# Performance work log

Measured on AMD Instinct MI355X. Metric: run time of the kernel, lower is better.

The kernel has to match this reference:

```python
import jax, jax.numpy as jnp
import numpy as np

NEG = -1e9

def setup_inputs() -> dict:
    key = jax.random.key(0)
    k1, k2, k3, k4, k5 = jax.random.split(key, 5)
    B, S, D = 4, 2048, 1024
    x = jax.random.normal(k1, (B, S, D), dtype=jnp.float32)
    Wq = jax.random.normal(k2, (D, D), dtype=jnp.float32) * (1.0 / np.sqrt(D))
    Wk = jax.random.normal(k3, (D, D), dtype=jnp.float32) * (1.0 / np.sqrt(D))
    Wv = jax.random.normal(k4, (D, D), dtype=jnp.float32) * (1.0 / np.sqrt(D))
    mask = jax.random.randint(k5, (B, S), 0, 2) > 0  # bool [B,S]
    return {"x": x, "Wq": Wq, "Wk": Wk, "Wv": Wv, "mask": mask}

def reference(x, Wq, Wk, Wv, mask):
    # x: [B,S,D]; single-head self-attention, scale = 1/sqrt(D)
    D = x.shape[-1]
    scale = 1.0 / D ** 0.5
    q = jnp.einsum('bsi,ij->bsj', x, Wq)
    k = jnp.einsum('bsi,ij->bsj', x, Wk)
    y = jnp.einsum('bsi,bzi->bsz', q, k) * scale  # [B,S,S]
    # additive mask: (~mask)[:, :, None] * -1e9 broadcasts over key axis
    m = (~mask).astype(jnp.float32)[:, :, None]
    y = y + m * NEG
    v = jnp.einsum('bsi,ij->bsj', x, Wv)
    attn = jax.nn.softmax(y, axis=-1)
    return jnp.einsum('bsz,bzi->bsi', attn, v)
```

## Files before the change

### kernel.cpp

```cpp
#include <hip/hip_runtime.h>

typedef __bf16 bf16x8 __attribute__((ext_vector_type(8)));
typedef float f32x4 __attribute__((ext_vector_type(4)));
typedef unsigned short u16;

__device__ __forceinline__ u16 f2bf(float f) {
    union { float f; unsigned u; } v; v.f = f;
    unsigned r = (v.u + 0x7FFFu + ((v.u >> 16) & 1u)) >> 16;
    return (u16)r;
}

__global__ __launch_bounds__(256)
void normMask(const unsigned int* __restrict__ m, unsigned char* __restrict__ nm) {
    __shared__ int isByte;
    if (threadIdx.x == 0) isByte = 0;
    __syncthreads();
    int bad = 0;
    for (int i = threadIdx.x; i < 2048; i += 256) bad |= (m[i] > 1u);
    if (bad) atomicOr(&isByte, 1);
    __syncthreads();
    if (isByte) {
        const unsigned char* mb = (const unsigned char*)m;
        for (int i = threadIdx.x; i < 8192; i += 256) nm[i] = mb[i] ? 1 : 0;
    } else {
        for (int i = threadIdx.x; i < 8192; i += 256) nm[i] = (unsigned char)m[i];
    }
}

__global__ __launch_bounds__(256)
void transW(const float* __restrict__ Wq, const float* __restrict__ Wk,
            const float* __restrict__ Wv, u16* __restrict__ Wt) {
    __shared__ u16 tile[64][65];
    const float* W = blockIdx.z == 0 ? Wq : (blockIdx.z == 1 ? Wk : Wv);
    u16* out = Wt + (size_t)blockIdx.z * 1024 * 1024;
    int k0 = blockIdx.x * 64, n0 = blockIdx.y * 64;
    int t = threadIdx.x, cl = t & 63, rw = t >> 6;
    #pragma unroll
    for (int r = 0; r < 16; ++r) {
        int row = r * 4 + rw;
        tile[cl][row] = f2bf(W[(size_t)(k0 + row) * 1024 + n0 + cl]);
    }
    __syncthreads();
    #pragma unroll
    for (int r = 0; r < 16; ++r) {
        int row = r * 4 + rw;
        out[(size_t)(n0 + row) * 1024 + k0 + cl] = tile[row][cl];
    }
}

__global__ __launch_bounds__(256)
void convX(const float* __restrict__ x, u16* __restrict__ xb) {
    const size_t n4 = (size_t)8192 * 1024 / 4;
    for (size_t i = (size_t)blockIdx.x * 256 + threadIdx.x; i < n4; i += (size_t)gridDim.x * 256) {
        float4 v = ((const float4*)x)[i];
        ushort4 o = make_ushort4(f2bf(v.x), f2bf(v.y), f2bf(v.z), f2bf(v.w));
        ((ushort4*)xb)[i] = o;
    }
}

__global__ __launch_bounds__(256)
void transV(const u16* __restrict__ qkv, u16* __restrict__ vt) {
    __shared__ u16 tile[64][65];
    int b = blockIdx.z;
    int s0 = blockIdx.x * 64, d0 = blockIdx.y * 64;
    int t = threadIdx.x, cl = t & 63, rw = t >> 6;
    const u16* src = qkv + (size_t)b * 2048 * 3072 + 2048;
    #pragma unroll
    for (int r = 0; r < 16; ++r) {
        int row = r * 4 + rw;
        tile[cl][row] = src[(size_t)(s0 + row) * 3072 + d0 + cl];
    }
    __syncthreads();
    u16* dst = vt + (size_t)b * 1024 * 2048;
    #pragma unroll
    for (int r = 0; r < 16; ++r) {
        int row = r * 4 + rw;
        dst[(size_t)(d0 + row) * 2048 + s0 + cl] = tile[row][cl];
    }
}

template <int OUTV>
__global__ __launch_bounds__(256, 2)
void gemm_bt(const u16* __restrict__ A0, int lda, size_t sA,
             const u16* __restrict__ B0, int ldb, size_t sB,
             void* __restrict__ Cout, int ldc, size_t sC, int kdim) {
    __shared__ u16 lA[128 * 64];
    __shared__ u16 lB[128 * 64];
    const u16* A = A0 + (size_t)blockIdx.z * sA;
    const u16* B = B0 + (size_t)blockIdx.z * sB;
    const int t = threadIdx.x;
    const int w = t >> 6, l = t & 63;
    const int wr = w >> 1, wc = w & 1;
    const int brow = blockIdx.x * 128, bcol = blockIdx.y * 128;
    const int rt = l >> 3;
    const int cb = (l & 7) * 8;

    auto ldsA3 = (__attribute__((address_space(3))) char*)lA;
    auto ldsB3 = (__attribute__((address_space(3))) char*)lB;

    f32x4 acc[4][4];
    #pragma unroll
    for (int m = 0; m < 4; ++m)
        #pragma unroll
        for (int n = 0; n < 4; ++n)
            acc[m][n] = (f32x4){0.f, 0.f, 0.f, 0.f};

    for (int k0 = 0; k0 < kdim; k0 += 64) {
        __syncthreads();
        #pragma unroll
        for (int p = 0; p < 4; ++p) {
            int chunk = p * 4 + w;
            const u16* ga = A + (size_t)(brow + chunk * 8 + rt) * lda + k0 + cb;
            __builtin_amdgcn_global_load_lds(
                (const __attribute__((address_space(1))) void*)ga,
                (__attribute__((address_space(3))) void*)(ldsA3 + chunk * 1024), 16, 0, 0);
            const u16* gb = B + (size_t)(bcol + chunk * 8 + rt) * ldb + k0 + cb;
            __builtin_amdgcn_global_load_lds(
                (const __attribute__((address_space(1))) void*)gb,
                (__attribute__((address_space(3))) void*)(ldsB3 + chunk * 1024), 16, 0, 0);
        }
        __syncthreads();
        #pragma unroll
        for (int kk = 0; kk < 2; ++kk) {
            bf16x8 af[4], bfv[4];
            #pragma unroll
            for (int m = 0; m < 4; ++m)
                af[m] = *(const bf16x8*)&lA[(wr * 64 + m * 16 + (l & 15)) * 64 + kk * 32 + (l >> 4) * 8];
            #pragma unroll
            for (int n = 0; n < 4; ++n)
                bfv[n] = *(const bf16x8*)&lB[(wc * 64 + n * 16 + (l & 15)) * 64 + kk * 32 + (l >> 4) * 8];
            #pragma unroll
            for (int m = 0; m < 4; ++m)
                #pragma unroll
                for (int n = 0; n < 4; ++n)
                    acc[m][n] = __builtin_amdgcn_mfma_f32_16x16x32_bf16(af[m], bfv[n], acc[m][n], 0, 0, 0);
        }
    }

    const int lrow = (l >> 4) * 4, lcol = l & 15;
    #pragma unroll
    for (int m = 0; m < 4; ++m) {
        #pragma unroll
        for (int n = 0; n < 4; ++n) {
            int rr = brow + wr * 64 + m * 16 + lrow;
            int cc = bcol + wc * 64 + n * 16 + lcol;
            #pragma unroll
            for (int j = 0; j < 4; ++j) {
                if constexpr (OUTV == 0)
                    ((u16*)Cout)[(size_t)blockIdx.z * sC + (size_t)(rr + j) * ldc + cc] = f2bf(acc[m][n][j]);
                else
                    ((float*)Cout)[(size_t)blockIdx.z * sC + (size_t)(rr + j) * ldc + cc] = acc[m][n][j];
            }
        }
    }
}

__global__ __launch_bounds__(256)
void softmax_rows(const float* __restrict__ S0, size_t sS, u16* __restrict__ P0, size_t sP,
                  const unsigned char* __restrict__ nm, int bbase) {
    const int row = blockIdx.x, t = threadIdx.x;
    const int b = bbase + blockIdx.z;
    const float* S = S0 + (size_t)blockIdx.z * sS;
    u16* dst = P0 + (size_t)blockIdx.z * sP + (size_t)row * 2048;
    if (nm[b * 2048 + row] == 0) {
        ushort4 u = make_ushort4(0x3A00, 0x3A00, 0x3A00, 0x3A00);
        ((ushort4*)dst)[t] = u;
        ((ushort4*)dst)[t + 256] = u;
        return;
    }
    const float4* src = (const float4*)(S + (size_t)row * 2048);
    float4 a = src[t], c = src[t + 256];
    float v[8] = {a.x, a.y, a.z, a.w, c.x, c.y, c.z, c.w};
    float mx = -1e30f;
    #pragma unroll
    for (int i = 0; i < 8; ++i) { v[i] *= 0.03125f; mx = fmaxf(mx, v[i]); }
    #pragma unroll
    for (int o = 32; o > 0; o >>= 1) mx = fmaxf(mx, __shfl_xor(mx, o));
    __shared__ float redm[4], reds[4];
    if ((t & 63) == 0) redm[t >> 6] = mx;
    __syncthreads();
    mx = fmaxf(fmaxf(redm[0], redm[1]), fmaxf(redm[2], redm[3]));
    float s = 0.f;
    #pragma unroll
    for (int i = 0; i < 8; ++i) { v[i] = expf(v[i] - mx); s += v[i]; }
    #pragma unroll
    for (int o = 32; o > 0; o >>= 1) s += __shfl_xor(s, o);
    if ((t & 63) == 0) reds[t >> 6] = s;
    __syncthreads();
    s = (reds[0] + reds[1]) + (reds[2] + reds[3]);
    float inv = 1.0f / s;
    ushort4 o0 = make_ushort4(f2bf(v[0] * inv), f2bf(v[1] * inv), f2bf(v[2] * inv), f2bf(v[3] * inv));
    ushort4 o1 = make_ushort4(f2bf(v[4] * inv), f2bf(v[5] * inv), f2bf(v[6] * inv), f2bf(v[7] * inv));
    ((ushort4*)dst)[t] = o0;
    ((ushort4*)dst)[t + 256] = o1;
}

extern "C" void kernel_launch(void* const* d_in, const int* in_sizes, int n_in,
                              void* d_out, int out_size, void* d_ws, size_t ws_size,
                              hipStream_t stream) {
    const float* x  = (const float*)d_in[0];
    const float* Wq = (const float*)d_in[1];
    const float* Wk = (const float*)d_in[2];
    const float* Wv = (const float*)d_in[3];
    const unsigned int* mask = (const unsigned int*)d_in[4];
    float* out = (float*)d_out;

    char* p = (char*)d_ws;
    u16* Wt  = (u16*)p;  p += (size_t)3072 * 1024 * 2;
    u16* xb  = (u16*)p;  p += (size_t)8192 * 1024 * 2;
    u16* qkv = (u16*)p;  p += (size_t)8192 * 3072 * 2;
    u16* vt  = (u16*)p;  p += (size_t)4 * 1024 * 2048 * 2;
    char* base = p;
    const size_t sizeS = (size_t)2048 * 2048 * 4;
    const size_t sizeP = (size_t)2048 * 2048 * 2;
    bool batched = ws_size >= (size_t)(base - (char*)d_ws) + 4 * (sizeS + sizeP) + 8192;

    float* S = (float*)base;
    u16* P;
    unsigned char* nm;
    if (batched) {
        P  = (u16*)(base + 4 * sizeS);
        nm = (unsigned char*)(base + 4 * (sizeS + sizeP));
    } else {
        P  = (u16*)(base + sizeS);
        nm = (unsigned char*)(base + sizeS + sizeP);
    }

    normMask<<<1, 256, 0, stream>>>(mask, nm);
    transW<<<dim3(16, 16, 3), 256, 0, stream>>>(Wq, Wk, Wv, Wt);
    convX<<<2048, 256, 0, stream>>>(x, xb);
    gemm_bt<0><<<dim3(64, 24, 1), 256, 0, stream>>>(xb, 1024, 0, Wt, 1024, 0, qkv, 3072, 0, 1024);
    transV<<<dim3(32, 16, 4), 256, 0, stream>>>(qkv, vt);
    if (batched) {
        gemm_bt<1><<<dim3(16, 16, 4), 256, 0, stream>>>(
            qkv, 3072, (size_t)2048 * 3072, qkv + 1024, 3072, (size_t)2048 * 3072,
            S, 2048, (size_t)2048 * 2048, 1024);
        softmax_rows<<<dim3(2048, 1, 4), 256, 0, stream>>>(
            S, (size_t)2048 * 2048, P, (size_t)2048 * 2048, nm, 0);
        gemm_bt<2><<<dim3(16, 8, 4), 256, 0, stream>>>(
            P, 2048, (size_t)2048 * 2048, vt, 2048, (size_t)1024 * 2048,
            out, 1024, (size_t)2048 * 1024, 2048);
    } else {
        for (int b = 0; b < 4; ++b) {
            const u16* Qb = qkv + (size_t)b * 2048 * 3072;
            gemm_bt<1><<<dim3(16, 16, 1), 256, 0, stream>>>(
                Qb, 3072, 0, Qb + 1024, 3072, 0, S, 2048, 0, 1024);
            softmax_rows<<<dim3(2048, 1, 1), 256, 0, stream>>>(S, 0, P, 0, nm, b);
            gemm_bt<2><<<dim3(16, 8, 1), 256, 0, stream>>>(
                P, 2048, 0, vt + (size_t)b * 1024 * 2048, 2048, 0,
                out + (size_t)b * 2048 * 1024, 1024, 0, 2048);
        }
    }
}
```

Measured before the change: 213.8 us.

## Add 256x256 8-wave GEMM with direct global-to-LDS loads for QKV and scores

Adds a new GEMM kernel that uses 256x256 tiles with 512 threads. It loads global data straight into LDS through the global_load_lds builtin, double-buffers the k-steps, and raises wave priority around the MFMA bursts. An optional block-index swizzle groups blocks for L2 locality. The kernel replaces the 128x128 gemm_bt for the QKV projection and the QK^T score GEMM, aiming for more data reuse per block and better overlap of loads with MFMA. In exchange it uses 128KB of LDS per block, and the tight waitcnt and barrier ordering it relies on is hard to get right.

Result: no change. 211.0 us (-1.3%).

```diff
diff --git a/kernel.cpp b/kernel.cpp
--- a/kernel.cpp
+++ b/kernel.cpp
@@ -8,6 +8,12 @@
     union { float f; unsigned u; } v; v.f = f;
     unsigned r = (v.u + 0x7FFFu + ((v.u >> 16) & 1u)) >> 16;
     return (u16)r;
+}
+
+__device__ __forceinline__ void fence_bar() {
+    asm volatile("" ::: "memory");
+    __builtin_amdgcn_s_barrier();
+    asm volatile("" ::: "memory");
 }
 
 __global__ __launch_bounds__(256)
@@ -76,6 +82,148 @@
     for (int r = 0; r < 16; ++r) {
         int row = r * 4 + rw;
         dst[(size_t)(d0 + row) * 2048 + s0 + cl] = tile[row][cl];
+    }
+}
+
+template <int OUTV, int SWZ>
+__global__ __launch_bounds__(512, 2)
+void gemm8p(const u16* __restrict__ A_, int lda, size_t sA,
+            const u16* __restrict__ B_, int ldb, size_t sB,
+            void* __restrict__ Cout, int ldc, size_t sC,
+            int kdim, int ntiles) {
+    __shared__ u16 lds[65536];
+    const u16* A = A_ + (size_t)blockIdx.z * sA;
+    const u16* B = B_ + (size_t)blockIdx.z * sB;
+
+    int bid = blockIdx.x;
+    if (SWZ) {
+        int cpx = gridDim.x >> 3;
+        bid = (bid & 7) * cpx + (bid >> 3);
+    }
+    const int brow = (bid / ntiles) * 256, bcol = (bid % ntiles) * 256;
+
+    const int t = threadIdx.x;
+    const int w = t >> 6, l = t & 63;
+    const int wr = w >> 2, wc = w & 3;
+
+    const size_t gA_th = (size_t)(brow + w * 16 + (l >> 2)) * lda + (l & 3) * 8;
+    const size_t gB_th = (size_t)(bcol + w * 16 + (l >> 2)) * ldb + (l & 3) * 8;
+    const int stTh = w * 512 + l * 8;
+    const int rA = (wr * 128 + (l & 15)) * 32 + (l >> 4) * 8;
+    const int rB = 32768 + (wc * 64 + (l & 15)) * 32 + (l >> 4) * 8;
+
+    auto lds3 = (__attribute__((address_space(3))) char*)lds;
+
+    #define ISSUE(matB, kk, tt, buf) do {                                          \
+        const u16* gp0 = ((matB) ? B : A) + ((matB) ? gB_th : gA_th)               \
+                         + (size_t)(tt) * 64 + (size_t)(kk) * 32;                  \
+        const int ldm_ = (matB) ? ldb : lda;                                       \
+        const int lbase_ = ((matB) ? 32768 : 0) + (buf) * 16384 + (kk) * 8192 + stTh; \
+        __builtin_amdgcn_global_load_lds(                                          \
+            (const __attribute__((address_space(1))) void*)gp0,                    \
+            (__attribute__((address_space(3))) void*)(lds3 + 2 * lbase_), 16, 0, 0); \
+        __builtin_amdgcn_global_load_lds(                                          \
+            (const __attribute__((address_space(1))) void*)(gp0 + (size_t)128 * ldm_), \
+            (__attribute__((address_space(3))) void*)(lds3 + 2 * (lbase_ + 4096)), 16, 0, 0); \
+    } while (0)
+
+    f32x4 acc[8][4];
+    #pragma unroll
+    for (int m = 0; m < 8; ++m)
+        #pragma unroll
+        for (int n = 0; n < 4; ++n)
+            acc[m][n] = (f32x4){0.f, 0.f, 0.f, 0.f};
+
+    const int NT = kdim >> 6;
+
+    ISSUE(0, 0, 0, 0); ISSUE(1, 0, 0, 0); ISSUE(0, 1, 0, 0); ISSUE(1, 1, 0, 0);
+    if (NT > 1) {
+        ISSUE(0, 0, 1, 1); ISSUE(1, 0, 1, 1);
+        asm volatile("s_waitcnt vmcnt(4)" ::: "memory");
+    } else {
+        asm volatile("s_waitcnt vmcnt(0)" ::: "memory");
+    }
+    fence_bar();
+
+    for (int tt = 0; tt < NT; ++tt) {
+        const int c = tt & 1;
+        const int ab = c * 16384;
+        bf16x8 af[4], bfv[4];
+
+        #pragma unroll
+        for (int m = 0; m < 4; ++m) af[m] = *(const bf16x8*)&lds[ab + rA + m * 512];
+        #pragma unroll
+        for (int n = 0; n < 4; ++n) bfv[n] = *(const bf16x8*)&lds[ab + rB + n * 512];
+        if (tt + 1 < NT) { ISSUE(0, 1, tt + 1, c ^ 1); ISSUE(1, 1, tt + 1, c ^ 1); }
+        fence_bar();
+        __builtin_amdgcn_s_setprio(1);
+        #pragma unroll
+        for (int m = 0; m < 4; ++m)
+            #pragma unroll
+            for (int n = 0; n < 4; ++n)
+                acc[m][n] = __builtin_amdgcn_mfma_f32_16x16x32_bf16(af[m], bfv[n], acc[m][n], 0, 0, 0);
+        __builtin_amdgcn_s_setprio(0);
+        fence_bar();
+
+        #pragma unroll
+        for (int m = 0; m < 4; ++m) af[m] = *(const bf16x8*)&lds[ab + rA + (m + 4) * 512];
+        fence_bar();
+        __builtin_amdgcn_s_setprio(1);
+        #pragma unroll
+        for (int m = 0; m < 4; ++m)
+            #pragma unroll
+            for (int n = 0; n < 4; ++n)
+                acc[m + 4][n] = __builtin_amdgcn_mfma_f32_16x16x32_bf16(af[m], bfv[n], acc[m + 4][n], 0, 0, 0);
+        __builtin_amdgcn_s_setprio(0);
+        fence_bar();
+
+        #pragma unroll
+        for (int m = 0; m < 4; ++m) af[m] = *(const bf16x8*)&lds[ab + 8192 + rA + m * 512];
+        #pragma unroll
+        for (int n = 0; n < 4; ++n) bfv[n] = *(const bf16x8*)&lds[ab + 8192 + rB + n * 512];
+        if (tt + 2 < NT) ISSUE(0, 0, tt + 2, c);
+        fence_bar();
+        __builtin_amdgcn_s_setprio(1);
+        #pragma unroll
+        for (int m = 0; m < 4; ++m)
+            #pragma unroll
+            for (int n = 0; n < 4; ++n)
+                acc[m][n] = __builtin_amdgcn_mfma_f32_16x16x32_bf16(af[m], bfv[n], acc[m][n], 0, 0, 0);
+        __builtin_amdgcn_s_setprio(0);
+        fence_bar();
+
+        #pragma unroll
+        for (int m = 0; m < 4; ++m) af[m] = *(const bf16x8*)&lds[ab + 8192 + rA + (m + 4) * 512];
+        if (tt + 2 < NT) ISSUE(1, 0, tt + 2, c);
+        fence_bar();
+        __builtin_amdgcn_s_setprio(1);
+        #pragma unroll
+        for (int m = 0; m < 4; ++m)
+            #pragma unroll
+            for (int n = 0; n < 4; ++n)
+                acc[m + 4][n] = __builtin_amdgcn_mfma_f32_16x16x32_bf16(af[m], bfv[n], acc[m + 4][n], 0, 0, 0);
+        __builtin_amdgcn_s_setprio(0);
+        if (tt + 2 < NT) asm volatile("s_waitcnt vmcnt(4)" ::: "memory");
+        else             asm volatile("s_waitcnt vmcnt(0)" ::: "memory");
+        fence_bar();
+    }
+    #undef ISSUE
+
+    const int lr = (l >> 4) * 4, lc = l & 15;
+    #pragma unroll
+    for (int m = 0; m < 8; ++m) {
+        #pragma unroll
+        for (int n = 0; n < 4; ++n) {
+            int rr = brow + wr * 128 + m * 16 + lr;
+            int cc = bcol + wc * 64 + n * 16 + lc;
+            #pragma unroll
+            for (int j = 0; j < 4; ++j) {
+                if constexpr (OUTV == 0)
+                    ((u16*)Cout)[(size_t)blockIdx.z * sC + (size_t)(rr + j) * ldc + cc] = f2bf(acc[m][n][j]);
+                else
+                    ((float*)Cout)[(size_t)blockIdx.z * sC + (size_t)(rr + j) * ldc + cc] = acc[m][n][j];
+            }
+        }
     }
 }
 
@@ -229,12 +377,14 @@
     normMask<<<1, 256, 0, stream>>>(mask, nm);
     transW<<<dim3(16, 16, 3), 256, 0, stream>>>(Wq, Wk, Wv, Wt);
     convX<<<2048, 256, 0, stream>>>(x, xb);
-    gemm_bt<0><<<dim3(64, 24, 1), 256, 0, stream>>>(xb, 1024, 0, Wt, 1024, 0, qkv, 3072, 0, 1024);
+    gemm8p<0, 1><<<dim3(384, 1, 1), 512, 0, stream>>>(
+        xb, 1024, 0, Wt, 1024, 0, qkv, 3072, 0, 1024, 12);
     transV<<<dim3(32, 16, 4), 256, 0, stream>>>(qkv, vt);
+
     if (batched) {
-        gemm_bt<1><<<dim3(16, 16, 4), 256, 0, stream>>>(
+        gemm8p<1, 0><<<dim3(64, 1, 4), 512, 0, stream>>>(
             qkv, 3072, (size_t)2048 * 3072, qkv + 1024, 3072, (size_t)2048 * 3072,
-            S, 2048, (size_t)2048 * 2048, 1024);
+            S, 2048, (size_t)2048 * 2048, 1024, 8);
         softmax_rows<<<dim3(2048, 1, 4), 256, 0, stream>>>(
             S, (size_t)2048 * 2048, P, (size_t)2048 * 2048, nm, 0);
         gemm_bt<2><<<dim3(16, 8, 4), 256, 0, stream>>>(
@@ -243,8 +393,8 @@
     } else {
         for (int b = 0; b < 4; ++b) {
             const u16* Qb = qkv + (size_t)b * 2048 * 3072;
-            gemm_bt<1><<<dim3(16, 16, 1), 256, 0, stream>>>(
-                Qb, 3072, 0, Qb + 1024, 3072, 0, S, 2048, 0, 1024);
+            gemm8p<1, 0><<<dim3(64, 1, 1), 512, 0, stream>>>(
+                Qb, 3072, 0, Qb + 1024, 3072, 0, S, 2048, 0, 1024, 8);
             softmax_rows<<<dim3(2048, 1, 1), 256, 0, stream>>>(S, 0, P, 0, nm, b);
             gemm_bt<2><<<dim3(16, 8, 1), 256, 0, stream>>>(
                 P, 2048, 0, vt + (size_t)b * 1024 * 2048, 2048, 0,
```
